# Kernel optimization log

Hardware: AMD Instinct MI355X
Metric: run time of the kernel (lower is better)

Reference implementation:

```python
import jax, jax.numpy as jnp
import numpy as np

N_NODES = 4096
IN_FEATURES = 256
N_HEADS = 8
N_HIDDEN = 32  # out_features // n_heads = 256 // 8
NEG_SLOPE = 0.2
MASK_FILL = -1e9


def setup_inputs() -> dict:
    key = jax.random.key(0)
    k_h, k_adj, k_w, k_a = jax.random.split(key, 4)
    h = jax.random.normal(k_h, (N_NODES, IN_FEATURES), dtype=jnp.float32)
    adj_mat = jax.random.randint(k_adj, (N_NODES, N_NODES, 1), 0, 2, dtype=jnp.int32)
    # linear: Linear(in_features, n_hidden*n_heads, bias=False) -> W: [in, H*F]
    W = jax.random.normal(k_w, (IN_FEATURES, N_HEADS * N_HIDDEN), dtype=jnp.float32) / np.sqrt(IN_FEATURES)
    # attn: Linear(2*n_hidden, 1, bias=False) -> a: [2*F]
    a = jax.random.normal(k_a, (2 * N_HIDDEN,), dtype=jnp.float32) / np.sqrt(2 * N_HIDDEN)
    return {"h": h, "adj_mat": adj_mat, "W": W, "a": a}


def reference(h, adj_mat, W, a):
    n = h.shape[0]
    # g: [n, H, F]
    g = (h @ W).reshape(n, N_HEADS, N_HIDDEN)
    # attn(concat(g_i, g_j)) == g_i . a[:F] + g_j . a[F:]  (decomposed, same math,
    # avoids materializing the O(N^2 * H * 2F) concat tensor of the torch code)
    a_src, a_dst = a[:N_HIDDEN], a[N_HIDDEN:]
    s_src = jnp.einsum('nhf,f->nh', g, a_src)  # [n, H]
    s_dst = jnp.einsum('nhf,f->nh', g, a_dst)  # [n, H]
    e = jax.nn.leaky_relu(s_src[:, None, :] + s_dst[None, :, :], negative_slope=NEG_SLOPE)  # [n, n, H]
    e = jnp.where(adj_mat == 0, MASK_FILL, e)  # adj_mat [n, n, 1] broadcasts over heads
    att = jax.nn.softmax(e, axis=1)  # softmax over source nodes j (dropout in eval mode = identity)
    out = jnp.einsum('ijh,jhf->ihf', att, g)  # [n, H, F]
    return out.reshape(n, N_HEADS * N_HIDDEN)  # is_concat=True
```

## Files before the change

kernel.cpp:

```cpp
#include <hip/hip_runtime.h>

#define NN 4096
#define FIN 256
#define CC 256
#define NH 8
#define NW32 (NN / 32)

typedef __attribute__((ext_vector_type(8))) short short8;
typedef __attribute__((ext_vector_type(4))) float f32x4;
typedef __attribute__((ext_vector_type(4))) unsigned int u32x4;

__device__ __forceinline__ unsigned cvtpk_bf16(float lo, float hi) {
  unsigned r;
  asm("v_cvt_pk_bf16_f32 %0, %1, %2" : "=v"(r) : "v"(lo), "v"(hi));
  return r;
}

__device__ __forceinline__ unsigned short bf16rn(float x) {
  unsigned int u = __builtin_bit_cast(unsigned int, x);
  u += 0x7fffu + ((u >> 16) & 1u);
  return (unsigned short)(u >> 16);
}

__device__ __forceinline__ void gl_lds16(const void* g, void* l) {
  __builtin_amdgcn_global_load_lds(
      (const __attribute__((address_space(1))) void*)g,
      (__attribute__((address_space(3))) void*)l, 16, 0, 0);
}

#define GROWS 8
#define GEMM_BLKS (NN / GROWS)
#define BP_BLKS (NN * NW32 / 256)
__global__ __launch_bounds__(256) void k_gemm(
    const float* __restrict__ h, const float* __restrict__ W,
    const float* __restrict__ a, const int* __restrict__ adj,
    unsigned int* __restrict__ adjb, unsigned short* __restrict__ gTs,
    float4* __restrict__ spack, float* __restrict__ dtc) {
  __shared__ float hs[GROWS][FIN];
  const int t = threadIdx.x;
  const int bx = blockIdx.x;

  if (bx >= GEMM_BLKS) {
    const int wid = (bx - GEMM_BLKS) * 256 + t;
    const int row = wid >> 7, wd = wid & 127;
    const int* src = adj + (size_t)row * NN + wd * 32;
    int4 v[8];
#pragma unroll
    for (int s = 0; s < 8; ++s) v[s] = *(const int4*)&src[s * 4];
    unsigned int bits = 0;
#pragma unroll
    for (int s = 0; s < 8; ++s) {
      bits |= (v[s].x ? 1u : 0u) << (s * 4 + 0);
      bits |= (v[s].y ? 1u : 0u) << (s * 4 + 1);
      bits |= (v[s].z ? 1u : 0u) << (s * 4 + 2);
      bits |= (v[s].w ? 1u : 0u) << (s * 4 + 3);
    }
    adjb[(size_t)row * NW32 + wd] = bits;
    return;
  }

  const int r0 = bx * GROWS;
#pragma unroll
  for (int idx = t; idx < GROWS * FIN / 4; idx += 256) {
    const int r = idx >> 6, c4 = idx & 63;
    *(float4*)&hs[r][c4 * 4] =
        *(const float4*)&h[(size_t)(r0 + r) * FIN + c4 * 4];
  }
  __syncthreads();
  const int c = t;
  float acc[GROWS];
#pragma unroll
  for (int r = 0; r < GROWS; ++r) acc[r] = 0.f;
  for (int k = 0; k < FIN; k += 4) {
    const float w0 = W[(size_t)(k + 0) * CC + c];
    const float w1 = W[(size_t)(k + 1) * CC + c];
    const float w2 = W[(size_t)(k + 2) * CC + c];
    const float w3 = W[(size_t)(k + 3) * CC + c];
#pragma unroll
    for (int r = 0; r < GROWS; ++r) {
      const float4 hv = *(const float4*)&hs[r][k];
      acc[r] += hv.x * w0 + hv.y * w1 + hv.z * w2 + hv.w * w3;
    }
  }
  const int f = c & 31, hh = c >> 5;
  const float aS = a[f], aD = a[32 + f];
  unsigned short gu[GROWS];
#pragma unroll
  for (int r = 0; r < GROWS; ++r) {
    float ps = acc[r] * aS, pd = acc[r] * aD;
#pragma unroll
    for (int m = 1; m < 32; m <<= 1) {
      ps += __shfl_xor(ps, m, 64);
      pd += __shfl_xor(pd, m, 64);
    }
    if (f == 0) {
      const int n = r0 + r;
      spack[(size_t)hh * NN + n] =
          make_float4(__expf(ps), __expf(0.2f * ps), 0.f, 0.f);
      float* dc = dtc + ((size_t)(n >> 5) * NH + hh) * 64 + (n & 31);
      dc[0] = __expf(pd);
      dc[32] = __expf(0.2f * pd);
    }
    gu[r] = bf16rn(acc[r]);
  }
  uint4 gv;
  gv.x = (unsigned)gu[0] | ((unsigned)gu[1] << 16);
  gv.y = (unsigned)gu[2] | ((unsigned)gu[3] << 16);
  gv.z = (unsigned)gu[4] | ((unsigned)gu[5] << 16);
  gv.w = (unsigned)gu[6] | ((unsigned)gu[7] << 16);
  const int jc = r0 >> 5, qq = (r0 >> 3) & 3;
  const int p = qq ^ ((c >> 1) & 3);
  *(uint4*)(gTs + ((size_t)jc * 1024 + c * 4 + p) * 8) = gv;
}

struct Buf {
  unsigned short gt[2][2048];
  float dt[2][2][2][32];
};

__global__ __launch_bounds__(256, 2) void k_attn(
    const unsigned int* __restrict__ adjb, const unsigned short* __restrict__ gTs,
    const float4* __restrict__ spack, const float* __restrict__ dtc,
    float* __restrict__ acc_ws, float* __restrict__ l_ws,
    float* __restrict__ out, const int splits, const int direct) {
  __shared__ Buf buf[2];

  const int lane = threadIdx.x & 63;
  const int w = threadIdx.x >> 6;
  const int il = lane & 15, q = lane >> 4;
  const int bx = blockIdx.x;
  const int sp = bx & (splits - 1);
  const int rest = bx / splits;
  const int hg = rest & 3;
  const int ib = rest >> 2;
  const int i0w = ib * 128 + w * 32;
  const int jrange = NN / splits, j0b = sp * jrange;
  const int c0 = j0b >> 5;

  float e1v[2][2], e2v[2][2];
#pragma unroll
  for (int hp = 0; hp < 2; ++hp)
#pragma unroll
    for (int it = 0; it < 2; ++it) {
      const float4 v = spack[(size_t)(hg * 2 + hp) * NN + i0w + it * 16 + il];
      e1v[hp][it] = v.x; e2v[hp][it] = v.y;
    }

  f32x4 acc[2][2][2];
  f32x4 lac[2][2];
#pragma unroll
  for (int hp = 0; hp < 2; ++hp)
#pragma unroll
    for (int it = 0; it < 2; ++it) {
#pragma unroll
      for (int r = 0; r < 4; ++r) lac[hp][it][r] = 0.f;
#pragma unroll
      for (int ft = 0; ft < 2; ++ft)
#pragma unroll
        for (int r = 0; r < 4; ++r) acc[hp][it][ft][r] = 0.f;
    }

  const short8 ones = {(short)0x3F80, (short)0x3F80, (short)0x3F80,
                       (short)0x3F80, (short)0x3F80, (short)0x3F80,
                       (short)0x3F80, (short)0x3F80};

  const unsigned long long* ab0 =
      (const unsigned long long*)(adjb + (size_t)(i0w + il) * NW32) +
      (j0b >> 6);
  const unsigned long long* ab1 =
      (const unsigned long long*)(adjb + (size_t)(i0w + 16 + il) * NW32) +
      (j0b >> 6);
  const int sh = q * 8;
  const int pswz = q ^ ((il >> 1) & 3);

  auto stage = [&](Buf* b, int jb) {
#pragma unroll
    for (int sub = 0; sub < 2; ++sub) {
      const unsigned short* src =
          gTs + ((size_t)(c0 + jb * 2 + sub) * 1024 + hg * 256 + w * 64) * 8;
      gl_lds16(src + (size_t)lane * 8, (char*)&b->gt[sub][0] + (w * 64) * 16);
    }
    if (w == 0) {
      const float* dsrc =
          dtc +
          ((size_t)(c0 + jb * 2 + (lane >> 5)) * NH + hg * 2 + ((lane >> 4) & 1)) *
              64 +
          ((lane >> 3) & 1) * 32 + (lane & 7) * 4;
      gl_lds16(dsrc, (char*)&b->dt[0][0][0][0]);
    }
  };

  const int nbuf = jrange / 64;
  stage(&buf[0], 0);
  unsigned long long pb0 = ab0[0], pb1 = ab1[0];
  __syncthreads();
  int cur = 0;

  for (int jb = 0; jb < nbuf; ++jb) {
    if (jb + 1 < nbuf) stage(&buf[cur ^ 1], jb + 1);
    const Buf* bc = &buf[cur];
    const unsigned int bl0[2] = {(unsigned int)pb0, (unsigned int)(pb0 >> 32)};
    const unsigned int bl1[2] = {(unsigned int)pb1, (unsigned int)(pb1 >> 32)};
    if (jb + 1 < nbuf) { pb0 = ab0[jb + 1]; pb1 = ab1[jb + 1]; }

#pragma unroll
    for (int sub = 0; sub < 2; ++sub) {
      float adf[2][8];
#pragma unroll
      for (int e = 0; e < 8; ++e) {
        adf[0][e] = (float)((bl0[sub] >> (sh + e)) & 1u);
        adf[1][e] = (float)((bl1[sub] >> (sh + e)) & 1u);
      }
#pragma unroll
      for (int hp = 0; hp < 2; ++hp) {
        float e1j[8], e2j[8];
        *(float4*)&e1j[0] = *(const float4*)&bc->dt[sub][hp][0][q * 8];
        *(float4*)&e1j[4] = *(const float4*)&bc->dt[sub][hp][0][q * 8 + 4];
        *(float4*)&e2j[0] = *(const float4*)&bc->dt[sub][hp][1][q * 8];
        *(float4*)&e2j[4] = *(const float4*)&bc->dt[sub][hp][1][q * 8 + 4];
        const int u0 = (hp * 32 + il) * 4 + pswz;
        const short8 b0 = *(const short8*)&bc->gt[sub][u0 * 8];
        const short8 b1 = *(const short8*)&bc->gt[sub][(u0 + 64) * 8];
#pragma unroll
        for (int it = 0; it < 2; ++it) {
          const float ei1 = e1v[hp][it], ei2 = e2v[hp][it];
          float wv[8];
#pragma unroll
          for (int e = 0; e < 8; ++e)
            wv[e] = fmaxf(ei1 * e1j[e], ei2 * e2j[e]) * adf[it][e];
          u32x4 uu;
#pragma unroll
          for (int m = 0; m < 4; ++m)
            uu[m] = cvtpk_bf16(wv[2 * m], wv[2 * m + 1]);
          const short8 afr = __builtin_bit_cast(short8, uu);
          acc[hp][it][0] = __builtin_amdgcn_mfma_f32_16x16x32_bf16(
              afr, b0, acc[hp][it][0], 0, 0, 0);
          acc[hp][it][1] = __builtin_amdgcn_mfma_f32_16x16x32_bf16(
              afr, b1, acc[hp][it][1], 0, 0, 0);
          lac[hp][it] = __builtin_amdgcn_mfma_f32_16x16x32_bf16(
              afr, ones, lac[hp][it], 0, 0, 0);
        }
      }
    }
    __syncthreads();
    cur ^= 1;
  }

  if (direct) {
#pragma unroll
    for (int hp = 0; hp < 2; ++hp) {
      const int hh = hg * 2 + hp;
#pragma unroll
      for (int it = 0; it < 2; ++it)
#pragma unroll
        for (int r = 0; r < 4; ++r) {
          const float inv = 1.f / lac[hp][it][r];
          const size_t irow = i0w + it * 16 + q * 4 + r;
#pragma unroll
          for (int ft = 0; ft < 2; ++ft)
            out[irow * CC + hh * 32 + ft * 16 + il] =
                acc[hp][it][ft][r] * inv;
        }
    }
  } else {
#pragma unroll
    for (int hp = 0; hp < 2; ++hp) {
      const int hh = hg * 2 + hp;
#pragma unroll
      for (int it = 0; it < 2; ++it)
#pragma unroll
        for (int r = 0; r < 4; ++r) {
          const size_t irow = i0w + it * 16 + q * 4 + r;
          if (il == 0)
            l_ws[((size_t)sp * NH + hh) * NN + irow] = lac[hp][it][r];
#pragma unroll
          for (int ft = 0; ft < 2; ++ft)
            acc_ws[((size_t)sp * NN + irow) * CC + hh * 32 + ft * 16 + il] =
                acc[hp][it][ft][r];
        }
    }
  }
}

__global__ __launch_bounds__(256) void k_combine(
    const float* __restrict__ acc_ws, const float* __restrict__ l_ws,
    float* __restrict__ out, const int splits) {
  const int idx = blockIdx.x * 256 + threadIdx.x;
  const int row = idx >> 6, c4 = idx & 63;
  const int hh = c4 >> 3;
  float ax = 0.f, ay = 0.f, az = 0.f, aw = 0.f, l = 0.f;
  for (int s = 0; s < splits; ++s) {
    const float4 v =
        *(const float4*)&acc_ws[((size_t)s * NN + row) * CC + c4 * 4];
    ax += v.x; ay += v.y; az += v.z; aw += v.w;
    l += l_ws[((size_t)s * NH + hh) * NN + row];
  }
  const float inv = 1.f / l;
  *(float4*)&out[(size_t)row * CC + c4 * 4] =
      make_float4(ax * inv, ay * inv, az * inv, aw * inv);
}

extern "C" void kernel_launch(void* const* d_in, const int* in_sizes, int n_in,
                              void* d_out, int out_size, void* d_ws,
                              size_t ws_size, hipStream_t stream) {
  (void)in_sizes; (void)n_in; (void)out_size;
  const float* h = (const float*)d_in[0];
  const int* adj = (const int*)d_in[1];
  const float* W = (const float*)d_in[2];
  const float* a = (const float*)d_in[3];
  float* out = (float*)d_out;
  char* ws = (char*)d_ws;

  unsigned short* gTs = (unsigned short*)ws;
  float4* spack = (float4*)(ws + (size_t)NN * CC * 2);
  float* dtc = (float*)(spack + (size_t)NH * NN);
  unsigned int* adjb =
      (unsigned int*)(dtc + (size_t)(NN / 32) * NH * 64);
  char* after = (char*)(adjb + (size_t)NN * NW32);
  const size_t base = (size_t)(after - ws);
  const size_t per_split = (size_t)NN * CC * 4 + (size_t)NH * NN * 4;

  int splits = 1;
  if (ws_size >= base + 8 * per_split) splits = 8;
  else if (ws_size >= base + 4 * per_split) splits = 4;
  else if (ws_size >= base + 2 * per_split) splits = 2;

  k_gemm<<<GEMM_BLKS + BP_BLKS, 256, 0, stream>>>(h, W, a, adj, adjb, gTs,
                                                  spack, dtc);

  const int nblk = (NN / 128) * 4 * splits;
  if (splits == 1) {
    k_attn<<<nblk, 256, 0, stream>>>(adjb, gTs, spack, dtc, nullptr, nullptr,
                                     out, 1, 1);
  } else {
    float* acc_ws = (float*)after;
    float* l_ws = acc_ws + (size_t)splits * NN * CC;
    k_attn<<<nblk, 256, 0, stream>>>(adjb, gTs, spack, dtc, acc_ws, l_ws, out,
                                     splits, 0);
    k_combine<<<NN * CC / 4 / 256, 256, 0, stream>>>(acc_ws, l_ws, out,
                                                     splits);
  }
}
```

Before: 69.73 us.

## Retile attention to one head per block with 256 rows and single-buffered 512-column stages

The attention kernel now gives each block one head and 256 destination rows (64 per wave) instead of two heads and 128 rows. It stages 512 source columns at a time into one shared buffer, with a sync before and after each load, replacing the 64-column double buffer. The dtc layout becomes head-major so each stage can read it as one contiguous run. Launch bounds go up to 3 blocks per SM. The intent is more reuse of each staged g tile across rows and fewer barriers, but loads no longer overlap compute, and the larger register tile may limit occupancy.

```diff
diff --git a/kernel.cpp b/kernel.cpp
--- a/kernel.cpp
+++ b/kernel.cpp
@@ -97,7 +97,7 @@
       const int n = r0 + r;
       spack[(size_t)hh * NN + n] =
           make_float4(__expf(ps), __expf(0.2f * ps), 0.f, 0.f);
-      float* dc = dtc + ((size_t)(n >> 5) * NH + hh) * 64 + (n & 31);
+      float* dc = dtc + ((size_t)hh * (NN / 32) + (n >> 5)) * 64 + (n & 31);
       dc[0] = __expf(pd);
       dc[32] = __expf(0.2f * pd);
     }
@@ -113,17 +113,13 @@
   *(uint4*)(gTs + ((size_t)jc * 1024 + c * 4 + p) * 8) = gv;
 }
 
-struct Buf {
-  unsigned short gt[2][2048];
-  float dt[2][2][2][32];
-};
-
-__global__ __launch_bounds__(256, 2) void k_attn(
+__global__ __launch_bounds__(256, 3) void k_attn(
     const unsigned int* __restrict__ adjb, const unsigned short* __restrict__ gTs,
     const float4* __restrict__ spack, const float* __restrict__ dtc,
     float* __restrict__ acc_ws, float* __restrict__ l_ws,
     float* __restrict__ out, const int splits, const int direct) {
-  __shared__ Buf buf[2];
+  __shared__ unsigned short gt_lds[2048 * 8];
+  __shared__ float dt_lds[16][2][32];
 
   const int lane = threadIdx.x & 63;
   const int w = threadIdx.x >> 6;
@@ -131,154 +127,143 @@
   const int bx = blockIdx.x;
   const int sp = bx & (splits - 1);
   const int rest = bx / splits;
-  const int hg = rest & 3;
-  const int ib = rest >> 2;
-  const int i0w = ib * 128 + w * 32;
+  const int hh = rest & 7;
+  const int ib = rest >> 3;
+  const int i0w = ib * 256 + w * 64;
   const int jrange = NN / splits, j0b = sp * jrange;
   const int c0 = j0b >> 5;
 
-  float e1v[2][2], e2v[2][2];
-#pragma unroll
-  for (int hp = 0; hp < 2; ++hp)
-#pragma unroll
-    for (int it = 0; it < 2; ++it) {
-      const float4 v = spack[(size_t)(hg * 2 + hp) * NN + i0w + it * 16 + il];
-      e1v[hp][it] = v.x; e2v[hp][it] = v.y;
-    }
-
-  f32x4 acc[2][2][2];
-  f32x4 lac[2][2];
-#pragma unroll
-  for (int hp = 0; hp < 2; ++hp)
-#pragma unroll
-    for (int it = 0; it < 2; ++it) {
-#pragma unroll
-      for (int r = 0; r < 4; ++r) lac[hp][it][r] = 0.f;
-#pragma unroll
-      for (int ft = 0; ft < 2; ++ft)
-#pragma unroll
-        for (int r = 0; r < 4; ++r) acc[hp][it][ft][r] = 0.f;
-    }
+  float e1v[4], e2v[4];
+#pragma unroll
+  for (int it = 0; it < 4; ++it) {
+    const float4 v = spack[(size_t)hh * NN + i0w + it * 16 + il];
+    e1v[it] = v.x; e2v[it] = v.y;
+  }
+
+  f32x4 acc[4][2];
+  f32x4 lac[4];
+#pragma unroll
+  for (int it = 0; it < 4; ++it) {
+#pragma unroll
+    for (int r = 0; r < 4; ++r) lac[it][r] = 0.f;
+#pragma unroll
+    for (int ft = 0; ft < 2; ++ft)
+#pragma unroll
+      for (int r = 0; r < 4; ++r) acc[it][ft][r] = 0.f;
+  }
 
   const short8 ones = {(short)0x3F80, (short)0x3F80, (short)0x3F80,
                        (short)0x3F80, (short)0x3F80, (short)0x3F80,
                        (short)0x3F80, (short)0x3F80};
 
-  const unsigned long long* ab0 =
-      (const unsigned long long*)(adjb + (size_t)(i0w + il) * NW32) +
-      (j0b >> 6);
-  const unsigned long long* ab1 =
-      (const unsigned long long*)(adjb + (size_t)(i0w + 16 + il) * NW32) +
-      (j0b >> 6);
+  const unsigned long long* ab[4];
+#pragma unroll
+  for (int it = 0; it < 4; ++it)
+    ab[it] = (const unsigned long long*)(adjb +
+                                         (size_t)(i0w + it * 16 + il) * NW32) +
+             (j0b >> 6);
+
   const int sh = q * 8;
   const int pswz = q ^ ((il >> 1) & 3);
 
-  auto stage = [&](Buf* b, int jb) {
-#pragma unroll
-    for (int sub = 0; sub < 2; ++sub) {
+  auto stage = [&](int s) {
+    const int jc0 = c0 + s * 16;
+#pragma unroll
+    for (int p = 0; p < 8; ++p) {
+      const int base = p * 256 + w * 64;
+      const int g = base + lane;
       const unsigned short* src =
-          gTs + ((size_t)(c0 + jb * 2 + sub) * 1024 + hg * 256 + w * 64) * 8;
-      gl_lds16(src + (size_t)lane * 8, (char*)&b->gt[sub][0] + (w * 64) * 16);
-    }
-    if (w == 0) {
+          gTs + (((size_t)(jc0 + (g >> 7)) << 10) + hh * 128 + (g & 127)) * 8;
+      gl_lds16(src, (char*)gt_lds + (size_t)base * 16);
+    }
+    {
+      const int base = w * 64;
       const float* dsrc =
-          dtc +
-          ((size_t)(c0 + jb * 2 + (lane >> 5)) * NH + hg * 2 + ((lane >> 4) & 1)) *
-              64 +
-          ((lane >> 3) & 1) * 32 + (lane & 7) * 4;
-      gl_lds16(dsrc, (char*)&b->dt[0][0][0][0]);
+          dtc + ((size_t)hh * (NN / 32) + jc0) * 64 + (base + lane) * 4;
+      gl_lds16(dsrc, (char*)&dt_lds[0][0][0] + (size_t)base * 16);
     }
   };
 
-  const int nbuf = jrange / 64;
-  stage(&buf[0], 0);
-  unsigned long long pb0 = ab0[0], pb1 = ab1[0];
-  __syncthreads();
-  int cur = 0;
-
-  for (int jb = 0; jb < nbuf; ++jb) {
-    if (jb + 1 < nbuf) stage(&buf[cur ^ 1], jb + 1);
-    const Buf* bc = &buf[cur];
-    const unsigned int bl0[2] = {(unsigned int)pb0, (unsigned int)(pb0 >> 32)};
-    const unsigned int bl1[2] = {(unsigned int)pb1, (unsigned int)(pb1 >> 32)};
-    if (jb + 1 < nbuf) { pb0 = ab0[jb + 1]; pb1 = ab1[jb + 1]; }
-
-#pragma unroll
-    for (int sub = 0; sub < 2; ++sub) {
-      float adf[2][8];
-#pragma unroll
-      for (int e = 0; e < 8; ++e) {
-        adf[0][e] = (float)((bl0[sub] >> (sh + e)) & 1u);
-        adf[1][e] = (float)((bl1[sub] >> (sh + e)) & 1u);
-      }
-#pragma unroll
-      for (int hp = 0; hp < 2; ++hp) {
+  const int nstg = jrange >> 9;
+  for (int s = 0; s < nstg; ++s) {
+    __syncthreads();
+    stage(s);
+    unsigned long long pb[4];
+#pragma unroll
+    for (int it = 0; it < 4; ++it) pb[it] = ab[it][s * 8];
+    __syncthreads();
+
+    for (int cp = 0; cp < 8; ++cp) {
+      unsigned int bl[4][2];
+#pragma unroll
+      for (int it = 0; it < 4; ++it) {
+        bl[it][0] = (unsigned int)pb[it];
+        bl[it][1] = (unsigned int)(pb[it] >> 32);
+      }
+      if (cp + 1 < 8) {
+#pragma unroll
+        for (int it = 0; it < 4; ++it) pb[it] = ab[it][s * 8 + cp + 1];
+      }
+#pragma unroll
+      for (int sub = 0; sub < 2; ++sub) {
+        const int ch = cp * 2 + sub;
         float e1j[8], e2j[8];
-        *(float4*)&e1j[0] = *(const float4*)&bc->dt[sub][hp][0][q * 8];
-        *(float4*)&e1j[4] = *(const float4*)&bc->dt[sub][hp][0][q * 8 + 4];
-        *(float4*)&e2j[0] = *(const float4*)&bc->dt[sub][hp][1][q * 8];
-        *(float4*)&e2j[4] = *(const float4*)&bc->dt[sub][hp][1][q * 8 + 4];
-        const int u0 = (hp * 32 + il) * 4 + pswz;
-        const short8 b0 = *(const short8*)&bc->gt[sub][u0 * 8];
-        const short8 b1 = *(const short8*)&bc->gt[sub][(u0 + 64) * 8];
-#pragma unroll
-        for (int it = 0; it < 2; ++it) {
-          const float ei1 = e1v[hp][it], ei2 = e2v[hp][it];
+        *(float4*)&e1j[0] = *(const float4*)&dt_lds[ch][0][q * 8];
+        *(float4*)&e1j[4] = *(const float4*)&dt_lds[ch][0][q * 8 + 4];
+        *(float4*)&e2j[0] = *(const float4*)&dt_lds[ch][1][q * 8];
+        *(float4*)&e2j[4] = *(const float4*)&dt_lds[ch][1][q * 8 + 4];
+        const int u0 = ch * 128 + il * 4 + pswz;
+        const short8 b0 = *(const short8*)&gt_lds[(size_t)u0 * 8];
+        const short8 b1 = *(const short8*)&gt_lds[(size_t)(u0 + 64) * 8];
+#pragma unroll
+        for (int it = 0; it < 4; ++it) {
+          const unsigned int bits = bl[it][sub];
+          const float ei1 = e1v[it], ei2 = e2v[it];
           float wv[8];
 #pragma unroll
           for (int e = 0; e < 8; ++e)
-            wv[e] = fmaxf(ei1 * e1j[e], ei2 * e2j[e]) * adf[it][e];
+            wv[e] = fmaxf(ei1 * e1j[e], ei2 * e2j[e]) *
+                    (float)((bits >> (sh + e)) & 1u);
           u32x4 uu;
 #pragma unroll
           for (int m = 0; m < 4; ++m)
             uu[m] = cvtpk_bf16(wv[2 * m], wv[2 * m + 1]);
           const short8 afr = __builtin_bit_cast(short8, uu);
-          acc[hp][it][0] = __builtin_amdgcn_mfma_f32_16x16x32_bf16(
-              afr, b0, acc[hp][it][0], 0, 0, 0);
-          acc[hp][it][1] = __builtin_amdgcn_mfma_f32_16x16x32_bf16(
-              afr, b1, acc[hp][it][1], 0, 0, 0);
-          lac[hp][it] = __builtin_amdgcn_mfma_f32_16x16x32_bf16(
-              afr, ones, lac[hp][it], 0, 0, 0);
+          acc[it][0] = __builtin_amdgcn_mfma_f32_16x16x32_bf16(
+              afr, b0, acc[it][0], 0, 0, 0);
+          acc[it][1] = __builtin_amdgcn_mfma_f32_16x16x32_bf16(
+              afr, b1, acc[it][1], 0, 0, 0);
+          lac[it] = __builtin_amdgcn_mfma_f32_16x16x32_bf16(
+              afr, ones, lac[it], 0, 0, 0);
         }
       }
     }
-    __syncthreads();
-    cur ^= 1;
   }
 
   if (direct) {
 #pragma unroll
-    for (int hp = 0; hp < 2; ++hp) {
-      const int hh = hg * 2 + hp;
-#pragma unroll
-      for (int it = 0; it < 2; ++it)
-#pragma unroll
-        for (int r = 0; r < 4; ++r) {
-          const float inv = 1.f / lac[hp][it][r];
-          const size_t irow = i0w + it * 16 + q * 4 + r;
-#pragma unroll
-          for (int ft = 0; ft < 2; ++ft)
-            out[irow * CC + hh * 32 + ft * 16 + il] =
-                acc[hp][it][ft][r] * inv;
-        }
-    }
+    for (int it = 0; it < 4; ++it)
+#pragma unroll
+      for (int r = 0; r < 4; ++r) {
+        const float inv = 1.f / lac[it][r];
+        const size_t irow = i0w + it * 16 + q * 4 + r;
+#pragma unroll
+        for (int ft = 0; ft < 2; ++ft)
+          out[irow * CC + hh * 32 + ft * 16 + il] = acc[it][ft][r] * inv;
+      }
   } else {
 #pragma unroll
-    for (int hp = 0; hp < 2; ++hp) {
-      const int hh = hg * 2 + hp;
-#pragma unroll
-      for (int it = 0; it < 2; ++it)
-#pragma unroll
-        for (int r = 0; r < 4; ++r) {
-          const size_t irow = i0w + it * 16 + q * 4 + r;
-          if (il == 0)
-            l_ws[((size_t)sp * NH + hh) * NN + irow] = lac[hp][it][r];
-#pragma unroll
-          for (int ft = 0; ft < 2; ++ft)
-            acc_ws[((size_t)sp * NN + irow) * CC + hh * 32 + ft * 16 + il] =
-                acc[hp][it][ft][r];
-        }
-    }
+    for (int it = 0; it < 4; ++it)
+#pragma unroll
+      for (int r = 0; r < 4; ++r) {
+        const size_t irow = i0w + it * 16 + q * 4 + r;
+        if (il == 0)
+          l_ws[((size_t)sp * NH + hh) * NN + irow] = lac[it][r];
+#pragma unroll
+        for (int ft = 0; ft < 2; ++ft)
+          acc_ws[((size_t)sp * NN + irow) * CC + hh * 32 + ft * 16 + il] =
+              acc[it][ft][r];
+      }
   }
 }
 
@@ -315,7 +300,7 @@
   float4* spack = (float4*)(ws + (size_t)NN * CC * 2);
   float* dtc = (float*)(spack + (size_t)NH * NN);
   unsigned int* adjb =
-      (unsigned int*)(dtc + (size_t)(NN / 32) * NH * 64);
+      (unsigned int*)(dtc + (size_t)NH * (NN / 32) * 64);
   char* after = (char*)(adjb + (size_t)NN * NW32);
   const size_t base = (size_t)(after - ws);
   const size_t per_split = (size_t)NN * CC * 4 + (size_t)NH * NN * 4;
@@ -328,7 +313,7 @@
   k_gemm<<<GEMM_BLKS + BP_BLKS, 256, 0, stream>>>(h, W, a, adj, adjb, gTs,
                                                   spack, dtc);
 
-  const int nblk = (NN / 128) * 4 * splits;
+  const int nblk = (NN / 256) * NH * splits;
   if (splits == 1) {
     k_attn<<<nblk, 256, 0, stream>>>(adjb, gTs, spack, dtc, nullptr, nullptr,
                                      out, 1, 1);
```

Measured after the change: 70.64 us. No clear change (+1.3%).
